# Optimization experiments

Measured on AMD Instinct MI355X. Metric: run time of the kernel, lower is better.

Reference implementation:

```python
import jax, jax.numpy as jnp
import numpy as np

B, N, D_IN, D_OUT = 4, 512, 128, 64
TEMP = 1.0
BN_EPS = 1e-5


def setup_inputs() -> dict:
    key = jax.random.key(0)
    ks = jax.random.split(key, 9)
    return {
        "x": jax.random.normal(ks[0], (B, N, D_IN), jnp.float32),
        "att_proj_w": jax.random.normal(ks[1], (D_OUT, D_IN), jnp.float32) * 0.08,
        "att_proj_b": jax.random.normal(ks[2], (D_OUT,), jnp.float32) * 0.01,
        "att_weight": jax.random.normal(ks[3], (D_OUT, 1), jnp.float32) * 0.15,
        "proj_with_att_w": jax.random.normal(ks[4], (D_OUT, D_IN), jnp.float32) * 0.08,
        "proj_with_att_b": jax.random.normal(ks[5], (D_OUT,), jnp.float32) * 0.01,
        "proj_without_att_w": jax.random.normal(ks[6], (D_OUT, D_IN), jnp.float32) * 0.08,
        "proj_without_att_b": jax.random.normal(ks[7], (D_OUT,), jnp.float32) * 0.01,
        "bn_gamma": jnp.ones((D_OUT,), jnp.float32),
        "bn_beta": jnp.zeros((D_OUT,), jnp.float32),
    }


def reference(x, att_proj_w, att_proj_b, att_weight,
              proj_with_att_w, proj_with_att_b,
              proj_without_att_w, proj_without_att_b,
              bn_gamma, bn_beta):
    # Dropout is identity (inference). Pairwise node multiplication: (B,N,N,D_in)
    pair = x[:, :, None, :] * x[:, None, :, :]
    # Linear + tanh on the pairwise tensor -> (B,N,N,D_out)
    a = jnp.tanh(jnp.einsum('bijd,od->bijo', pair, att_proj_w) + att_proj_b)
    # Score via learned vector, temperature, softmax over second node axis (torch dim=-2 of (B,N,N,1))
    scores = jnp.einsum('bijo,o->bij', a, att_weight[:, 0]) / TEMP
    att = jax.nn.softmax(scores, axis=2)  # normalize over j
    # Attention-weighted aggregation + two projections (torch Linear: x @ W.T + b)
    agg = jnp.einsum('bij,bjd->bid', att, x)
    h = (agg @ proj_with_att_w.T + proj_with_att_b) \
        + (x @ proj_without_att_w.T + proj_without_att_b)
    # BatchNorm1d (training-mode batch stats) over flattened (B*N, D_out)
    hf = h.reshape(-1, h.shape[-1])
    mean = hf.mean(axis=0)
    var = hf.var(axis=0)  # biased, as torch BN uses for normalization
    y = (hf - mean) / jnp.sqrt(var + BN_EPS) * bn_gamma + bn_beta
    y = y.reshape(h.shape)
    return jax.nn.selu(y)
```

## Files before the change

### kernel.cpp

```cpp
#include <hip/hip_runtime.h>
#include <math.h>

#define NB 4
#define NN 512
#define DIN 128
#define DOUT 64
#define TI 2
#define CHROWS 32
#define NCH (NN / CHROWS)

typedef __attribute__((ext_vector_type(8))) short short8;
typedef __attribute__((ext_vector_type(8))) unsigned short ushort8;
typedef __attribute__((ext_vector_type(4))) float f32x4;

__device__ __forceinline__ unsigned short f2bf(float f) {
    union { float f; unsigned u; } v; v.f = f;
    unsigned r = v.u + 0x7fffu + ((v.u >> 16) & 1u);
    return (unsigned short)(r >> 16);
}

__device__ __forceinline__ float bf2f(unsigned short u) {
    union { unsigned u; float f; } v; v.u = ((unsigned)u) << 16; return v.f;
}

__global__ void x_to_bf16(const float* __restrict__ x, unsigned short* __restrict__ xbf) {
    const int idx = blockIdx.x * 256 + threadIdx.x;
    float4 v = ((const float4*)x)[idx];
    ushort4 o;
    o.x = f2bf(v.x); o.y = f2bf(v.y); o.z = f2bf(v.z); o.w = f2bf(v.w);
    ((ushort4*)xbf)[idx] = o;
}

__global__ __launch_bounds__(512, 4) void gat_main(
    const float* __restrict__ x,
    const unsigned short* __restrict__ xbf,
    const float* __restrict__ apw,
    const float* __restrict__ apb,
    const float* __restrict__ attw,
    const float* __restrict__ pww,
    const float* __restrict__ pwb,
    const float* __restrict__ pow_,
    const float* __restrict__ pob,
    float* __restrict__ out)
{
    __shared__ unsigned short xt[2][CHROWS * DIN];
    __shared__ float scp[4][TI][NN];
    __shared__ float xis[TI][DIN];
    __shared__ float aw_s[DOUT];
    __shared__ float ab_s[DOUT];
    __shared__ float red_s[8][TI];
    __shared__ float bcs[TI];

    float* pagg = (float*)&xt[0][0];
    float* aggs = pagg + 8 * TI * DIN;
    float* pr   = aggs + TI * DIN;

    const int t = threadIdx.x;
    const int blk = blockIdx.x;
    const int b = blk >> 8;
    const int rowbase = (blk & 255) * TI;
    const float* xb = x + (size_t)b * NN * DIN;
    const unsigned short* xbb = xbf + (size_t)b * NN * DIN;

    if (t < TI * DIN) {
        int i = t >> 7, d = t & 127;
        xis[i][d] = xb[(size_t)(rowbase + i) * DIN + d];
    }
    if (t < 64) { aw_s[t] = attw[t]; ab_s[t] = apb[t]; }
    __syncthreads();

    const int lane = t & 63, wid = t >> 6;
    const int og = wid & 3;
    const int jsub = wid >> 2;
    const int lr = lane & 15;
    const int g = lane >> 4;
    const int g8 = g * 8;

    const int st_row = t >> 4, st_gr = t & 15;
    const int st_off = st_row * 256 + ((st_gr ^ (st_row & 7)) << 4);
    const int rloc = jsub * 16 + lr;
    int rdoff[4];
    #pragma unroll
    for (int ks = 0; ks < 4; ++ks)
        rdoff[ks] = rloc * 256 + ((((ks * 4 + g) ^ (lr & 7))) << 4);

    ushort8 v0 = ((const ushort8*)xbb)[t];

    short8 afr[TI][4];
    {
        const float* wrow = apw + (size_t)(og * 16 + lr) * DIN;
        #pragma unroll
        for (int ks = 0; ks < 4; ++ks) {
            float4 w0 = *(const float4*)(wrow + ks * 32 + g8);
            float4 w1 = *(const float4*)(wrow + ks * 32 + g8 + 4);
            #pragma unroll
            for (int i = 0; i < TI; ++i) {
                const float* xk = &xis[i][ks * 32 + g8];
                short8 fr;
                fr[0] = (short)f2bf(w0.x * xk[0]);
                fr[1] = (short)f2bf(w0.y * xk[1]);
                fr[2] = (short)f2bf(w0.z * xk[2]);
                fr[3] = (short)f2bf(w0.w * xk[3]);
                fr[4] = (short)f2bf(w1.x * xk[4]);
                fr[5] = (short)f2bf(w1.y * xk[5]);
                fr[6] = (short)f2bf(w1.z * xk[6]);
                fr[7] = (short)f2bf(w1.w * xk[7]);
                afr[i][ks] = fr;
            }
        }
    }

    const float C2 = 2.885390081777927f;
    float awm2[4], abc[4], sumw = 0.0f;
    #pragma unroll
    for (int r = 0; r < 4; ++r) {
        const int o = og * 16 + g * 4 + r;
        float w = aw_s[o];
        awm2[r] = -2.0f * w;
        abc[r] = ab_s[o] * C2;
        sumw += w;
    }

    *(ushort8*)((char*)&xt[0][0] + st_off) = v0;
    __syncthreads();

    int p = 0;
    f32x4 accP[TI];
    #pragma unroll 2
    for (int ch = 0; ch < NCH; ++ch) {
        ushort8 vnext;
        if (ch + 1 < NCH) vnext = ((const ushort8*)xbb)[(ch + 1) * (CHROWS * DIN / 8) + t];

        short8 bfr[4];
        #pragma unroll
        for (int ks = 0; ks < 4; ++ks)
            bfr[ks] = *(const short8*)((const char*)&xt[p][0] + rdoff[ks]);

        f32x4 accC[TI];
        #pragma unroll
        for (int i = 0; i < TI; ++i) {
            f32x4 acc = {0.f, 0.f, 0.f, 0.f};
            #pragma unroll
            for (int ks = 0; ks < 4; ++ks)
                acc = __builtin_amdgcn_mfma_f32_16x16x32_bf16(afr[i][ks], bfr[ks], acc, 0, 0, 0);
            accC[i] = acc;
        }

        if (ch > 0) {
            const int jp = (ch - 1) * CHROWS + jsub * 16;
            float sp[TI];
            #pragma unroll
            for (int i = 0; i < TI; ++i) {
                float s = sumw;
                #pragma unroll
                for (int r = 0; r < 4; ++r) {
                    float arg = fmaf(accP[i][r], C2, abc[r]);
                    float u, rc;
                    asm("v_exp_f32 %0, %1" : "=v"(u) : "v"(arg));
                    float den = u + 1.0f;
                    asm("v_rcp_f32 %0, %1" : "=v"(rc) : "v"(den));
                    s = fmaf(awm2[r], rc, s);
                }
                sp[i] = s;
            }
            #pragma unroll
            for (int i = 0; i < TI; ++i) sp[i] += __shfl_xor(sp[i], 16);
            #pragma unroll
            for (int i = 0; i < TI; ++i) sp[i] += __shfl_xor(sp[i], 32);
            if (lane < 16) {
                #pragma unroll
                for (int i = 0; i < TI; ++i) scp[og][i][jp + lane] = sp[i];
            }
        }

        if (ch + 1 < NCH)
            *(ushort8*)((char*)&xt[p ^ 1][0] + st_off) = vnext;
        __syncthreads();
        #pragma unroll
        for (int i = 0; i < TI; ++i) accP[i] = accC[i];
        p ^= 1;
    }
    {
        const int jp = (NCH - 1) * CHROWS + jsub * 16;
        float sp[TI];
        #pragma unroll
        for (int i = 0; i < TI; ++i) {
            float s = sumw;
            #pragma unroll
            for (int r = 0; r < 4; ++r) {
                float arg = fmaf(accP[i][r], C2, abc[r]);
                float u, rc;
                asm("v_exp_f32 %0, %1" : "=v"(u) : "v"(arg));
                float den = u + 1.0f;
                asm("v_rcp_f32 %0, %1" : "=v"(rc) : "v"(den));
                s = fmaf(awm2[r], rc, s);
            }
            sp[i] = s;
        }
        #pragma unroll
        for (int i = 0; i < TI; ++i) sp[i] += __shfl_xor(sp[i], 16);
        #pragma unroll
        for (int i = 0; i < TI; ++i) sp[i] += __shfl_xor(sp[i], 32);
        if (lane < 16) {
            #pragma unroll
            for (int i = 0; i < TI; ++i) scp[og][i][jp + lane] = sp[i];
        }
    }
    __syncthreads();

    float s0 = scp[0][0][t] + scp[1][0][t] + scp[2][0][t] + scp[3][0][t];
    float s1 = scp[0][1][t] + scp[1][1][t] + scp[2][1][t] + scp[3][1][t];
    float e0 = __expf(s0), e1 = __expf(s1);
    float ss0 = e0, ss1 = e1;
    #pragma unroll
    for (int msk = 1; msk < 64; msk <<= 1) {
        ss0 += __shfl_xor(ss0, msk);
        ss1 += __shfl_xor(ss1, msk);
    }
    if (lane == 0) { red_s[wid][0] = ss0; red_s[wid][1] = ss1; }
    __syncthreads();
    scp[0][0][t] = e0;
    scp[0][1][t] = e1;
    if (t < TI) {
        float sm = 0.f;
        #pragma unroll
        for (int w = 0; w < 8; ++w) sm += red_s[w][t];
        bcs[t] = 1.0f / sm;
    }
    __syncthreads();

    const float* esc0 = &scp[0][0][0];
    const float* esc1 = &scp[0][1][0];
    {
        const int d0 = (t & 63) * 2, q = t >> 6;
        const unsigned short* xc = xbb + d0;
        float a00 = 0.f, a01 = 0.f, a10 = 0.f, a11 = 0.f;
        #pragma unroll 4
        for (int jj = q * 64; jj < q * 64 + 64; ++jj) {
            ushort2 xv = *(const ushort2*)(xc + (size_t)jj * DIN);
            float x0 = bf2f(xv.x), x1 = bf2f(xv.y);
            float e0v = esc0[jj], e1v = esc1[jj];
            a00 = fmaf(e0v, x0, a00); a01 = fmaf(e0v, x1, a01);
            a10 = fmaf(e1v, x0, a10); a11 = fmaf(e1v, x1, a11);
        }
        pagg[(q * TI + 0) * DIN + d0] = a00;
        pagg[(q * TI + 0) * DIN + d0 + 1] = a01;
        pagg[(q * TI + 1) * DIN + d0] = a10;
        pagg[(q * TI + 1) * DIN + d0 + 1] = a11;
    }
    __syncthreads();
    if (t < TI * DIN) {
        const int i = t >> 7, d = t & 127;
        float s = 0.f;
        #pragma unroll
        for (int q = 0; q < 8; ++q) s += pagg[(q * TI + i) * DIN + d];
        aggs[i * DIN + d] = s * bcs[i];
    }
    __syncthreads();

    {
        const int o = t & 63, pi = t >> 6;
        const int i = pi >> 2, part = pi & 3;
        const float* w1 = pww + (size_t)o * DIN + part * 32;
        const float* w2 = pow_ + (size_t)o * DIN + part * 32;
        const float* ag = aggs + i * DIN + part * 32;
        const float* xr = &xis[i][part * 32];
        float sum = 0.0f;
        #pragma unroll
        for (int dd = 0; dd < 32; ++dd)
            sum += w1[dd] * ag[dd] + w2[dd] * xr[dd];
        pr[pi * DOUT + o] = sum;
    }
    __syncthreads();
    if (t < TI * DOUT) {
        const int i = t >> 6, o = t & 63;
        float h = pr[(i * 4 + 0) * DOUT + o] + pr[(i * 4 + 1) * DOUT + o] +
                  pr[(i * 4 + 2) * DOUT + o] + pr[(i * 4 + 3) * DOUT + o] +
                  pwb[o] + pob[o];
        out[(size_t)(b * NN + rowbase + i) * DOUT + o] = h;
    }
}

__global__ void bn_stats(const float* __restrict__ h, float* __restrict__ stats) {
    const int c = blockIdx.x;
    const int t = threadIdx.x;
    float s = 0.f, s2 = 0.f;
    for (int r = t; r < NB * NN; r += 256) {
        float v = h[(size_t)r * DOUT + c];
        s += v; s2 += v * v;
    }
    __shared__ float rs[256], rs2[256];
    rs[t] = s; rs2[t] = s2;
    __syncthreads();
    for (int k = 128; k > 0; k >>= 1) {
        if (t < k) { rs[t] += rs[t + k]; rs2[t] += rs2[t + k]; }
        __syncthreads();
    }
    if (t == 0) {
        const float inv_n = 1.0f / (float)(NB * NN);
        float mean = rs[0] * inv_n;
        float var = rs2[0] * inv_n - mean * mean;
        stats[c] = mean;
        stats[DOUT + c] = rsqrtf(var + 1e-5f);
    }
}

__global__ void bn_selu(float* __restrict__ out, const float* __restrict__ stats,
                        const float* __restrict__ gamma, const float* __restrict__ beta) {
    const int idx = blockIdx.x * 256 + threadIdx.x;
    const int c = idx & 63;
    float v = out[idx];
    float y = (v - stats[c]) * stats[DOUT + c] * gamma[c] + beta[c];
    const float scale = 1.0507009873554805f;
    const float alpha = 1.6732632423543772f;
    out[idx] = y > 0.0f ? scale * y : scale * alpha * (__expf(y) - 1.0f);
}

extern "C" void kernel_launch(void* const* d_in, const int* in_sizes, int n_in,
                              void* d_out, int out_size, void* d_ws, size_t ws_size,
                              hipStream_t stream) {
    const float* x    = (const float*)d_in[0];
    const float* apw  = (const float*)d_in[1];
    const float* apb  = (const float*)d_in[2];
    const float* attw = (const float*)d_in[3];
    const float* pww  = (const float*)d_in[4];
    const float* pwb  = (const float*)d_in[5];
    const float* pow_ = (const float*)d_in[6];
    const float* pob  = (const float*)d_in[7];
    const float* gmm  = (const float*)d_in[8];
    const float* bta  = (const float*)d_in[9];
    float* out = (float*)d_out;
    float* stats = (float*)d_ws;
    unsigned short* xbf = (unsigned short*)((char*)d_ws + 1024);

    x_to_bf16<<<256, 256, 0, stream>>>(x, xbf);
    gat_main<<<NB * NN / TI, 512, 0, stream>>>(x, xbf, apw, apb, attw, pww, pwb, pow_, pob, out);
    bn_stats<<<DOUT, 256, 0, stream>>>(out, stats);
    bn_selu<<<(NB * NN * DOUT) / 256, 256, 0, stream>>>(out, stats, gmm, bta);
}
```

Measured before the change: 71.95 us.

## Process four query rows per block and restructure the chunk pipeline

Doubles the number of query rows per block, so each staged bf16 chunk of x is reused across four rows' MFMA products and the grid halves to 512 blocks. The score buffer is transposed to [og][j][row] so four scores move with one vector store and load, and the main loop is rewritten as an explicit ping-pong with separate COMPUTE/POST lambdas. The aggregation and projection stages are re-split for four rows. The cost is more registers for A fragments and accumulators and fewer blocks, which may lower occupancy or leave CUs idle.

```diff
diff --git a/kernel.cpp b/kernel.cpp
--- a/kernel.cpp
+++ b/kernel.cpp
@@ -5,7 +5,7 @@
 #define NN 512
 #define DIN 128
 #define DOUT 64
-#define TI 2
+#define TI 4
 #define CHROWS 32
 #define NCH (NN / CHROWS)
 
@@ -44,30 +44,26 @@
     float* __restrict__ out)
 {
     __shared__ unsigned short xt[2][CHROWS * DIN];
-    __shared__ float scp[4][TI][NN];
+    __shared__ float scp[4][NN][TI];
     __shared__ float xis[TI][DIN];
-    __shared__ float aw_s[DOUT];
-    __shared__ float ab_s[DOUT];
     __shared__ float red_s[8][TI];
     __shared__ float bcs[TI];
 
     float* pagg = (float*)&xt[0][0];
-    float* aggs = pagg + 8 * TI * DIN;
+    float* aggs = &scp[1][0][0];
     float* pr   = aggs + TI * DIN;
 
     const int t = threadIdx.x;
     const int blk = blockIdx.x;
-    const int b = blk >> 8;
-    const int rowbase = (blk & 255) * TI;
+    const int b = blk >> 7;
+    const int rowbase = (blk & 127) * TI;
     const float* xb = x + (size_t)b * NN * DIN;
     const unsigned short* xbb = xbf + (size_t)b * NN * DIN;
 
-    if (t < TI * DIN) {
-        int i = t >> 7, d = t & 127;
+    {
+        const int i = t >> 7, d = t & 127;
         xis[i][d] = xb[(size_t)(rowbase + i) * DIN + d];
     }
-    if (t < 64) { aw_s[t] = attw[t]; ab_s[t] = apb[t]; }
-    __syncthreads();
 
     const int lane = t & 63, wid = t >> 6;
     const int og = wid & 3;
@@ -76,15 +72,16 @@
     const int g = lane >> 4;
     const int g8 = g * 8;
 
-    const int st_row = t >> 4, st_gr = t & 15;
-    const int st_off = st_row * 256 + ((st_gr ^ (st_row & 7)) << 4);
+    const int strow = t >> 4, stgr = t & 15;
+    const int st_off = strow * 256 + ((stgr ^ (strow & 7)) << 4);
     const int rloc = jsub * 16 + lr;
     int rdoff[4];
     #pragma unroll
     for (int ks = 0; ks < 4; ++ks)
-        rdoff[ks] = rloc * 256 + ((((ks * 4 + g) ^ (lr & 7))) << 4);
+        rdoff[ks] = rloc * 256 + (((ks * 4 + g) ^ (rloc & 7)) << 4);
 
     ushort8 v0 = ((const ushort8*)xbb)[t];
+    __syncthreads();
 
     short8 afr[TI][4];
     {
@@ -115,80 +112,38 @@
     #pragma unroll
     for (int r = 0; r < 4; ++r) {
         const int o = og * 16 + g * 4 + r;
-        float w = aw_s[o];
-        awm2[r] = -2.0f * w;
-        abc[r] = ab_s[o] * C2;
-        sumw += w;
+        float wv = attw[o], bv = apb[o];
+        awm2[r] = -2.0f * wv;
+        abc[r] = bv * C2;
+        sumw += wv;
     }
 
     *(ushort8*)((char*)&xt[0][0] + st_off) = v0;
     __syncthreads();
 
-    int p = 0;
-    f32x4 accP[TI];
-    #pragma unroll 2
-    for (int ch = 0; ch < NCH; ++ch) {
-        ushort8 vnext;
-        if (ch + 1 < NCH) vnext = ((const ushort8*)xbb)[(ch + 1) * (CHROWS * DIN / 8) + t];
-
-        short8 bfr[4];
-        #pragma unroll
-        for (int ks = 0; ks < 4; ++ks)
-            bfr[ks] = *(const short8*)((const char*)&xt[p][0] + rdoff[ks]);
-
-        f32x4 accC[TI];
-        #pragma unroll
-        for (int i = 0; i < TI; ++i) {
-            f32x4 acc = {0.f, 0.f, 0.f, 0.f};
-            #pragma unroll
-            for (int ks = 0; ks < 4; ++ks)
-                acc = __builtin_amdgcn_mfma_f32_16x16x32_bf16(afr[i][ks], bfr[ks], acc, 0, 0, 0);
-            accC[i] = acc;
-        }
-
-        if (ch > 0) {
-            const int jp = (ch - 1) * CHROWS + jsub * 16;
-            float sp[TI];
-            #pragma unroll
-            for (int i = 0; i < TI; ++i) {
-                float s = sumw;
-                #pragma unroll
-                for (int r = 0; r < 4; ++r) {
-                    float arg = fmaf(accP[i][r], C2, abc[r]);
-                    float u, rc;
-                    asm("v_exp_f32 %0, %1" : "=v"(u) : "v"(arg));
-                    float den = u + 1.0f;
-                    asm("v_rcp_f32 %0, %1" : "=v"(rc) : "v"(den));
-                    s = fmaf(awm2[r], rc, s);
-                }
-                sp[i] = s;
-            }
-            #pragma unroll
-            for (int i = 0; i < TI; ++i) sp[i] += __shfl_xor(sp[i], 16);
-            #pragma unroll
-            for (int i = 0; i < TI; ++i) sp[i] += __shfl_xor(sp[i], 32);
-            if (lane < 16) {
-                #pragma unroll
-                for (int i = 0; i < TI; ++i) scp[og][i][jp + lane] = sp[i];
-            }
-        }
-
-        if (ch + 1 < NCH)
-            *(ushort8*)((char*)&xt[p ^ 1][0] + st_off) = vnext;
-        __syncthreads();
-        #pragma unroll
-        for (int i = 0; i < TI; ++i) accP[i] = accC[i];
-        p ^= 1;
-    }
-    {
-        const int jp = (NCH - 1) * CHROWS + jsub * 16;
+    f32x4 accA[TI], accB[TI];
+
+    auto COMPUTE = [&](f32x4 (&acc)[TI], const int buf) {
+        #pragma unroll
+        for (int i = 0; i < TI; ++i) acc[i] = f32x4{0.f, 0.f, 0.f, 0.f};
+        #pragma unroll
+        for (int ks = 0; ks < 4; ++ks) {
+            short8 bk = *(const short8*)((const char*)&xt[buf][0] + rdoff[ks]);
+            #pragma unroll
+            for (int i = 0; i < TI; ++i)
+                acc[i] = __builtin_amdgcn_mfma_f32_16x16x32_bf16(afr[i][ks], bk, acc[i], 0, 0, 0);
+        }
+    };
+
+    auto POST = [&](f32x4 (&acc)[TI], const int ch) {
+        const int jp = ch * CHROWS + jsub * 16;
         float sp[TI];
         #pragma unroll
         for (int i = 0; i < TI; ++i) {
             float s = sumw;
             #pragma unroll
             for (int r = 0; r < 4; ++r) {
-                float arg = fmaf(accP[i][r], C2, abc[r]);
+                float arg = fmaf(acc[i][r], C2, abc[r]);
                 float u, rc;
                 asm("v_exp_f32 %0, %1" : "=v"(u) : "v"(arg));
                 float den = u + 1.0f;
@@ -202,25 +157,56 @@
         #pragma unroll
         for (int i = 0; i < TI; ++i) sp[i] += __shfl_xor(sp[i], 32);
         if (lane < 16) {
-            #pragma unroll
-            for (int i = 0; i < TI; ++i) scp[og][i][jp + lane] = sp[i];
-        }
-    }
-    __syncthreads();
-
-    float s0 = scp[0][0][t] + scp[1][0][t] + scp[2][0][t] + scp[3][0][t];
-    float s1 = scp[0][1][t] + scp[1][1][t] + scp[2][1][t] + scp[3][1][t];
-    float e0 = __expf(s0), e1 = __expf(s1);
-    float ss0 = e0, ss1 = e1;
-    #pragma unroll
-    for (int msk = 1; msk < 64; msk <<= 1) {
-        ss0 += __shfl_xor(ss0, msk);
-        ss1 += __shfl_xor(ss1, msk);
-    }
-    if (lane == 0) { red_s[wid][0] = ss0; red_s[wid][1] = ss1; }
-    __syncthreads();
-    scp[0][0][t] = e0;
-    scp[0][1][t] = e1;
+            f32x4 v = {sp[0], sp[1], sp[2], sp[3]};
+            *(f32x4*)&scp[og][jp + lane][0] = v;
+        }
+    };
+
+    {
+        ushort8 vn = ((const ushort8*)xbb)[1 * 512 + t];
+        COMPUTE(accA, 0);
+        *(ushort8*)((char*)&xt[1][0] + st_off) = vn;
+        __syncthreads();
+    }
+    for (int cb = 1; cb <= NCH - 3; cb += 2) {
+        {
+            ushort8 vn = ((const ushort8*)xbb)[(cb + 1) * 512 + t];
+            COMPUTE(accB, 1);
+            POST(accA, cb - 1);
+            *(ushort8*)((char*)&xt[0][0] + st_off) = vn;
+            __syncthreads();
+        }
+        {
+            ushort8 vn = ((const ushort8*)xbb)[(cb + 2) * 512 + t];
+            COMPUTE(accA, 0);
+            POST(accB, cb);
+            *(ushort8*)((char*)&xt[1][0] + st_off) = vn;
+            __syncthreads();
+        }
+    }
+    COMPUTE(accB, 1);
+    POST(accA, NCH - 2);
+    POST(accB, NCH - 1);
+    __syncthreads();
+
+    {
+        f32x4 s4 = *(const f32x4*)&scp[0][t][0];
+        s4 += *(const f32x4*)&scp[1][t][0];
+        s4 += *(const f32x4*)&scp[2][t][0];
+        s4 += *(const f32x4*)&scp[3][t][0];
+        float e0 = __expf(s4[0]), e1 = __expf(s4[1]), e2 = __expf(s4[2]), e3 = __expf(s4[3]);
+        f32x4 ev = {e0, e1, e2, e3};
+        *(f32x4*)&scp[0][t][0] = ev;
+        float ss[TI] = {e0, e1, e2, e3};
+        #pragma unroll
+        for (int msk = 1; msk < 64; msk <<= 1)
+            #pragma unroll
+            for (int i = 0; i < TI; ++i) ss[i] += __shfl_xor(ss[i], msk);
+        if (lane == 0)
+            #pragma unroll
+            for (int i = 0; i < TI; ++i) red_s[wid][i] = ss[i];
+    }
+    __syncthreads();
     if (t < TI) {
         float sm = 0.f;
         #pragma unroll
@@ -229,27 +215,29 @@
     }
     __syncthreads();
 
-    const float* esc0 = &scp[0][0][0];
-    const float* esc1 = &scp[0][1][0];
     {
         const int d0 = (t & 63) * 2, q = t >> 6;
         const unsigned short* xc = xbb + d0;
-        float a00 = 0.f, a01 = 0.f, a10 = 0.f, a11 = 0.f;
-        #pragma unroll 4
+        float a0[TI] = {0.f, 0.f, 0.f, 0.f};
+        float a1[TI] = {0.f, 0.f, 0.f, 0.f};
         for (int jj = q * 64; jj < q * 64 + 64; ++jj) {
             ushort2 xv = *(const ushort2*)(xc + (size_t)jj * DIN);
             float x0 = bf2f(xv.x), x1 = bf2f(xv.y);
-            float e0v = esc0[jj], e1v = esc1[jj];
-            a00 = fmaf(e0v, x0, a00); a01 = fmaf(e0v, x1, a01);
-            a10 = fmaf(e1v, x0, a10); a11 = fmaf(e1v, x1, a11);
-        }
-        pagg[(q * TI + 0) * DIN + d0] = a00;
-        pagg[(q * TI + 0) * DIN + d0 + 1] = a01;
-        pagg[(q * TI + 1) * DIN + d0] = a10;
-        pagg[(q * TI + 1) * DIN + d0 + 1] = a11;
-    }
-    __syncthreads();
-    if (t < TI * DIN) {
+            const f32x4 ev = *(const f32x4*)&scp[0][jj][0];
+            #pragma unroll
+            for (int i = 0; i < TI; ++i) {
+                a0[i] = fmaf(ev[i], x0, a0[i]);
+                a1[i] = fmaf(ev[i], x1, a1[i]);
+            }
+        }
+        #pragma unroll
+        for (int i = 0; i < TI; ++i) {
+            pagg[(q * TI + i) * DIN + d0] = a0[i];
+            pagg[(q * TI + i) * DIN + d0 + 1] = a1[i];
+        }
+    }
+    __syncthreads();
+    {
         const int i = t >> 7, d = t & 127;
         float s = 0.f;
         #pragma unroll
@@ -260,23 +248,21 @@
 
     {
         const int o = t & 63, pi = t >> 6;
-        const int i = pi >> 2, part = pi & 3;
-        const float* w1 = pww + (size_t)o * DIN + part * 32;
-        const float* w2 = pow_ + (size_t)o * DIN + part * 32;
-        const float* ag = aggs + i * DIN + part * 32;
-        const float* xr = &xis[i][part * 32];
+        const int i = pi >> 1, part = pi & 1;
+        const float* w1 = pww + (size_t)o * DIN + part * 64;
+        const float* w2 = pow_ + (size_t)o * DIN + part * 64;
+        const float* ag = aggs + i * DIN + part * 64;
+        const float* xr = &xis[i][part * 64];
         float sum = 0.0f;
         #pragma unroll
-        for (int dd = 0; dd < 32; ++dd)
+        for (int dd = 0; dd < 64; ++dd)
             sum += w1[dd] * ag[dd] + w2[dd] * xr[dd];
         pr[pi * DOUT + o] = sum;
     }
     __syncthreads();
     if (t < TI * DOUT) {
         const int i = t >> 6, o = t & 63;
-        float h = pr[(i * 4 + 0) * DOUT + o] + pr[(i * 4 + 1) * DOUT + o] +
-                  pr[(i * 4 + 2) * DOUT + o] + pr[(i * 4 + 3) * DOUT + o] +
-                  pwb[o] + pob[o];
+        float h = pr[(i * 2) * DOUT + o] + pr[(i * 2 + 1) * DOUT + o] + pwb[o] + pob[o];
         out[(size_t)(b * NN + rowbase + i) * DOUT + o] = h;
     }
 }
```

Result: slower. 88.05 us (+22.4%).
